# Performance work log

Measured on AMD Instinct MI355X. Metric: run time of the kernel, lower is better.

Reference implementation:

```python
import jax, jax.numpy as jnp
import numpy as np

N = 50_000      # nodes
E = 1_600_000   # edges (avg degree 32)
IN = 128        # in_channels
H = 128         # hidden_channels
OUT = 10        # out_channels
EA = 16         # edge_attr_channels


def setup_inputs() -> dict:
    key = jax.random.key(0)
    ks = jax.random.split(key, 16)
    def lin(k, fan_in, fan_out):
        return jax.random.normal(k, (fan_in, fan_out), dtype=jnp.float32) * (1.0 / np.sqrt(fan_in))
    return {
        "x": jax.random.normal(ks[0], (N, IN), dtype=jnp.float32),
        "edge_index": jax.random.randint(ks[1], (2, E), 0, N, dtype=jnp.int32),
        "edge_attr": jax.random.normal(ks[2], (E, EA), dtype=jnp.float32),
        # edge encoder MLP: Linear(EA->H) -> ReLU -> Linear(H->1)
        "We1": lin(ks[3], EA, H), "be1": jnp.zeros((H,), jnp.float32),
        "We2": lin(ks[4], H, 1),  "be2": jnp.zeros((1,), jnp.float32),
        # three GCNConv layers (in->H, H->H, H->H)
        "W1": lin(ks[5], IN, H), "b1": jnp.zeros((H,), jnp.float32),
        "W2": lin(ks[6], H, H),  "b2": jnp.zeros((H,), jnp.float32),
        "W3": lin(ks[7], H, H),  "b3": jnp.zeros((H,), jnp.float32),
        # head Linear(H->OUT)
        "Wh": lin(ks[8], H, OUT), "bh": jnp.zeros((OUT,), jnp.float32),
    }


def reference(x, edge_index, edge_attr, We1, be1, We2, be2,
              W1, b1, W2, b2, W3, b3, Wh, bh):
    n = x.shape[0]
    src, dst = edge_index[0], edge_index[1]

    # edge weight = softplus(MLP(edge_attr)).squeeze(-1)
    hidden = jax.nn.relu(edge_attr @ We1 + be1)          # [E, H]
    ew = jax.nn.softplus((hidden @ We2 + be2)[:, 0])      # [E]

    # add self-loops with weight 1 (GCNConv default)
    loops = jnp.arange(n, dtype=src.dtype)
    src_f = jnp.concatenate([src, loops])
    dst_f = jnp.concatenate([dst, loops])
    w_f = jnp.concatenate([ew, jnp.ones((n,), ew.dtype)])

    # symmetric normalization: D^{-1/2} A D^{-1/2}
    deg = jax.ops.segment_sum(w_f, dst_f, num_segments=n)   # [N]
    dis = jax.lax.rsqrt(jnp.maximum(deg, 1e-12))
    norm = dis[src_f] * w_f * dis[dst_f]                     # [E+N]

    def gcn_conv(h, W, b):
        h = h @ W                                             # [N, H]
        msg = norm[:, None] * h[src_f]                        # gather + scale
        agg = jax.ops.segment_sum(msg, dst_f, num_segments=n) # scatter-add
        return agg + b

    h = jax.nn.relu(gcn_conv(x, W1, b1))   # dropout is identity in eval
    h = jax.nn.relu(gcn_conv(h, W2, b2))
    h = jax.nn.relu(gcn_conv(h, W3, b3))

    graph_emb = jnp.mean(h, axis=0)        # global mean pool (single graph)
    return graph_emb @ Wh + bh             # [OUT], already squeezed
```

## Files before the change

kernel.cpp:

```cpp
#include <hip/hip_runtime.h>


#define HD   128
#define EAD  16
#define OUTD 10
#define PCHUNK 4096
#define PBLK 400

typedef short bf16x8 __attribute__((ext_vector_type(8)));
typedef float f32x16 __attribute__((ext_vector_type(16)));

static inline int ceil_div(long long a, long long b){ return (int)((a + b - 1) / b); }

__device__ inline unsigned f2bf(float f) {
    unsigned u = __float_as_uint(f);
    return (u + 0x7fffu + ((u >> 16) & 1u)) >> 16;
}
__device__ inline float bf_lo(unsigned w) { return __uint_as_float(w << 16); }
__device__ inline float bf_hi(unsigned w) { return __uint_as_float(w & 0xffff0000u); }

__device__ inline unsigned short f2h(float f) {
    _Float16 h = (_Float16)f;
    return __builtin_bit_cast(unsigned short, h);
}
__device__ inline float h2f(unsigned u) {
    _Float16 h = __builtin_bit_cast(_Float16, (unsigned short)(u & 0xffffu));
    return (float)h;
}
__device__ inline unsigned cvtpk(float lo, float hi) {
    unsigned r;
    asm volatile("v_cvt_pk_bf16_f32 %0, %1, %2" : "=v"(r) : "v"(lo), "v"(hi));
    return r;
}
__device__ inline unsigned relu_pk(unsigned w) {
    return w & ~(((w >> 15) & 0x10001u) * 0xFFFFu);
}
__device__ inline float softplus_fast(float v) {
    float t = __builtin_amdgcn_exp2f(-fabsf(v) * 1.44269504088896f);
    return fmaxf(v, 0.f) + 0.693147180559945f * __builtin_amdgcn_logf(1.0f + t);
}

__global__ __launch_bounds__(256) void k_edge_mlp(
    const float* __restrict__ edge_attr, const int* __restrict__ dst,
    const float* __restrict__ We1, const float* __restrict__ be1,
    const float* __restrict__ We2, const float* __restrict__ be2,
    float* __restrict__ ew, int* __restrict__ batom, int E, int NB)
{
    __shared__ int hist[256];
    const int tid = threadIdx.x;
    hist[tid] = 0;
    __syncthreads();

    const int lane = tid & 63;
    const int half = lane >> 5;
    const int lc   = lane & 31;
    const int wid  = blockIdx.x * 4 + (tid >> 6);
    const int nw   = gridDim.x * 4;
    const int G    = (E + 31) >> 5;

    bf16x8 bfr[4];
    bf16x8 abias[4];
    bf16x8 bones;
    bf16x8 we2A[8];
#pragma unroll
    for (int t = 0; t < 4; ++t) {
#pragma unroll
        for (int j = 0; j < 8; ++j) {
            int k = 4 * half + (j & 3) + 8 * (j >> 2);
            bfr[t][j]   = (short)f2bf(We1[k * HD + t * 32 + lc]);
            abias[t][j] = (half == 0 && j == 0) ? (short)f2bf(be1[t * 32 + lc]) : (short)0;
        }
    }
#pragma unroll
    for (int j = 0; j < 8; ++j)
        bones[j] = (half == 0 && j == 0) ? (short)0x3F80 : (short)0;
#pragma unroll
    for (int s = 0; s < 8; ++s)
#pragma unroll
        for (int j = 0; j < 8; ++j) {
            int k = 4 * half + (j & 3) + 8 * (j >> 2);
            we2A[s][j] = (short)f2bf(We2[s * 16 + k]);
        }
    const float be2v = be2[0];

    for (int g = wid * 2; g < G; g += nw * 2) {
        int g1 = g + 1;
        bool h1 = (g1 < G);
        int e0 = (g << 5) + lc;
        int e1 = h1 ? ((g1 << 5) + lc) : e0;
        int el0 = e0 < E ? e0 : E - 1;
        int el1 = e1 < E ? e1 : E - 1;
        bool own0 = (half == 0) && (e0 < E);
        bool own1 = h1 && (half == 0) && (e1 < E);
        if (own0) atomicAdd(&hist[((unsigned)dst[e0]) >> 8], 1);
        if (own1) atomicAdd(&hist[((unsigned)dst[e1]) >> 8], 1);

        const float4* r0 = reinterpret_cast<const float4*>(edge_attr + (size_t)el0 * EAD);
        const float4* r1 = reinterpret_cast<const float4*>(edge_attr + (size_t)el1 * EAD);
        float4 x00 = r0[half], x01 = r0[2 + half];
        float4 x10 = r1[half], x11 = r1[2 + half];
        union { uint2 u[2]; bf16x8 v; } af0, af1;
        af0.u[0] = make_uint2(cvtpk(x00.x, x00.y), cvtpk(x00.z, x00.w));
        af0.u[1] = make_uint2(cvtpk(x01.x, x01.y), cvtpk(x01.z, x01.w));
        af1.u[0] = make_uint2(cvtpk(x10.x, x10.y), cvtpk(x10.z, x10.w));
        af1.u[1] = make_uint2(cvtpk(x11.x, x11.y), cvtpk(x11.z, x11.w));

        f32x16 preA, preB;
#pragma unroll
        for (int i = 0; i < 16; ++i) { preA[i] = 0.f; preB[i] = 0.f; }
#pragma unroll
        for (int t = 0; t < 4; ++t) {
            f32x16 accA, accB;
#pragma unroll
            for (int i = 0; i < 16; ++i) { accA[i] = 0.f; accB[i] = 0.f; }
            accA = __builtin_amdgcn_mfma_f32_32x32x16_bf16(abias[t], bones, accA, 0, 0, 0);
            accB = __builtin_amdgcn_mfma_f32_32x32x16_bf16(abias[t], bones, accB, 0, 0, 0);
            accA = __builtin_amdgcn_mfma_f32_32x32x16_bf16(bfr[t], af0.v, accA, 0, 0, 0);
            accB = __builtin_amdgcn_mfma_f32_32x32x16_bf16(bfr[t], af1.v, accB, 0, 0, 0);
            union { uint2 u[2]; bf16x8 v; } ploA, phiA, ploB, phiB;
            ploA.u[0] = make_uint2(cvtpk(fmaxf(accA[0], 0.f),  fmaxf(accA[1], 0.f)),
                                   cvtpk(fmaxf(accA[2], 0.f),  fmaxf(accA[3], 0.f)));
            ploA.u[1] = make_uint2(cvtpk(fmaxf(accA[4], 0.f),  fmaxf(accA[5], 0.f)),
                                   cvtpk(fmaxf(accA[6], 0.f),  fmaxf(accA[7], 0.f)));
            phiA.u[0] = make_uint2(cvtpk(fmaxf(accA[8], 0.f),  fmaxf(accA[9], 0.f)),
                                   cvtpk(fmaxf(accA[10], 0.f), fmaxf(accA[11], 0.f)));
            phiA.u[1] = make_uint2(cvtpk(fmaxf(accA[12], 0.f), fmaxf(accA[13], 0.f)),
                                   cvtpk(fmaxf(accA[14], 0.f), fmaxf(accA[15], 0.f)));
            ploB.u[0] = make_uint2(cvtpk(fmaxf(accB[0], 0.f),  fmaxf(accB[1], 0.f)),
                                   cvtpk(fmaxf(accB[2], 0.f),  fmaxf(accB[3], 0.f)));
            ploB.u[1] = make_uint2(cvtpk(fmaxf(accB[4], 0.f),  fmaxf(accB[5], 0.f)),
                                   cvtpk(fmaxf(accB[6], 0.f),  fmaxf(accB[7], 0.f)));
            phiB.u[0] = make_uint2(cvtpk(fmaxf(accB[8], 0.f),  fmaxf(accB[9], 0.f)),
                                   cvtpk(fmaxf(accB[10], 0.f), fmaxf(accB[11], 0.f)));
            phiB.u[1] = make_uint2(cvtpk(fmaxf(accB[12], 0.f), fmaxf(accB[13], 0.f)),
                                   cvtpk(fmaxf(accB[14], 0.f), fmaxf(accB[15], 0.f)));
            preA = __builtin_amdgcn_mfma_f32_32x32x16_bf16(we2A[2*t],     ploA.v, preA, 0, 0, 0);
            preB = __builtin_amdgcn_mfma_f32_32x32x16_bf16(we2A[2*t],     ploB.v, preB, 0, 0, 0);
            preA = __builtin_amdgcn_mfma_f32_32x32x16_bf16(we2A[2*t + 1], phiA.v, preA, 0, 0, 0);
            preB = __builtin_amdgcn_mfma_f32_32x32x16_bf16(we2A[2*t + 1], phiB.v, preB, 0, 0, 0);
        }
        float v0 = preA[0] + be2v;
        float v1 = preB[0] + be2v;
        if (own0) ew[e0] = softplus_fast(v0);
        if (own1) ew[e1] = softplus_fast(v1);
    }
    __syncthreads();
    if (tid < NB && hist[tid]) atomicAdd(&batom[tid], hist[tid]);
}

__global__ __launch_bounds__(256) void k_bscan(
    const int* __restrict__ batom, int* __restrict__ boff,
    int* __restrict__ bcur, int NB)
{
    __shared__ int sh[256];
    int t = threadIdx.x;
    int v = (t < NB) ? batom[t] : 0;
    sh[t] = v;
    __syncthreads();
    for (int off = 1; off < 256; off <<= 1) {
        int add = (t >= off) ? sh[t - off] : 0;
        __syncthreads();
        sh[t] += add;
        __syncthreads();
    }
    if (t < NB) { boff[t] = sh[t] - v; bcur[t] = sh[t] - v; }
    if (t == NB - 1) boff[NB] = sh[t];
}

__global__ __launch_bounds__(256) void k_part(
    const int* __restrict__ src, const int* __restrict__ dst,
    const float* __restrict__ ew, int* __restrict__ bcur,
    uint2* __restrict__ bbuf, int E, int NB)
{
    __shared__ int hist[256];
    __shared__ int base[256];
    __shared__ int cur[256];
    int t = threadIdx.x;
    hist[t] = 0; cur[t] = 0;
    __syncthreads();
    int eb = blockIdx.x * PCHUNK;
#pragma unroll
    for (int k = 0; k < PCHUNK / 256; ++k) {
        int e = eb + k * 256 + t;
        if (e < E) atomicAdd(&hist[dst[e] >> 8], 1);
    }
    __syncthreads();
    if (t < NB && hist[t]) base[t] = atomicAdd(&bcur[t], hist[t]);
    __syncthreads();
#pragma unroll
    for (int k = 0; k < PCHUNK / 256; ++k) {
        int e = eb + k * 256 + t;
        if (e >= E) continue;
        int d = dst[e];
        int bkt = d >> 8;
        int pos = base[bkt] + atomicAdd(&cur[bkt], 1);
        bbuf[pos] = make_uint2(((unsigned)src[e] << 16) | f2h(ew[e]),
                               (unsigned)(d & 255));
    }
}

__global__ __launch_bounds__(256) void k_bucket(
    const int* __restrict__ boff, const uint2* __restrict__ bbuf,
    int* __restrict__ rp, float* __restrict__ dis,
    unsigned* __restrict__ adj, int N, int E, int NB)
{
    __shared__ int   hcnt[256];
    __shared__ int   hexc[256];
    __shared__ int   cur[256];
    __shared__ float degs[256];
    int b = blockIdx.x;
    int t = threadIdx.x;
    hcnt[t] = 0; cur[t] = 0; degs[t] = 0.f;
    __syncthreads();
    int beg = boff[b], end = boff[b + 1];
    for (int i = beg + t; i < end; i += 256) {
        uint2 ent = bbuf[i];
        int dl = (int)ent.y;
        atomicAdd(&hcnt[dl], 1);
        atomicAdd(&degs[dl], h2f(ent.x));
    }
    __syncthreads();
    {
        int v = hcnt[t];
        hexc[t] = v;
        __syncthreads();
        for (int off = 1; off < 256; off <<= 1) {
            int add = (t >= off) ? hexc[t - off] : 0;
            __syncthreads();
            hexc[t] += add;
            __syncthreads();
        }
        hexc[t] -= v;
    }
    int n = (b << 8) + t;
    if (n < N) {
        rp[n]  = beg + hexc[t];
        dis[n] = rsqrtf(fmaxf(1.0f + degs[t], 1e-12f));
    }
    if (b == NB - 1 && t == 0) rp[N] = E;
    __syncthreads();
    for (int i = beg + t; i < end; i += 256) {
        uint2 ent = bbuf[i];
        int dl = (int)ent.y;
        int pos = beg + hexc[dl] + atomicAdd(&cur[dl], 1);
        adj[pos] = ent.x;
    }
}

template <bool BF16IN, bool RELU>
__global__ __launch_bounds__(256) void k_gemm(
    const void* __restrict__ Xv, const float* __restrict__ W,
    const float* __restrict__ dis, unsigned short* __restrict__ Ybf, int N)
{
    __shared__ unsigned short Wt[128][132];
    int t = threadIdx.x;
#pragma unroll
    for (int i = 0; i < 64; ++i) {
        int e = i * 256 + t;
        int k = e >> 7, n = e & 127;
        Wt[n][k] = (unsigned short)f2bf(W[e]);
    }
    __syncthreads();

    const int lane = t & 63;
    const int half = lane >> 5;
    const int lc   = lane & 31;
    const int wid  = blockIdx.x * 4 + (t >> 6);
    const int nw   = gridDim.x * 4;
    const int T    = (N + 31) >> 5;

    for (int tile = wid; tile < T; tile += nw) {
        int rbase = tile << 5;
        int arow  = rbase + lc; if (arow >= N) arow = N - 1;

        f32x16 acc[4];
#pragma unroll
        for (int tb = 0; tb < 4; ++tb)
#pragma unroll
            for (int i = 0; i < 16; ++i) acc[tb][i] = 0.f;

#pragma unroll
        for (int kk = 0; kk < 8; ++kk) {
            union { uint2 u[2]; bf16x8 v; } af;
            if (BF16IN) {
                const unsigned short* Xb = (const unsigned short*)Xv;
                const unsigned short* rp = Xb + (size_t)arow * HD + kk * 16 + 4 * half;
                uint2 lo = *reinterpret_cast<const uint2*>(rp);
                uint2 hi = *reinterpret_cast<const uint2*>(rp + 8);
                if (RELU) {
                    lo.x = relu_pk(lo.x); lo.y = relu_pk(lo.y);
                    hi.x = relu_pk(hi.x); hi.y = relu_pk(hi.y);
                }
                af.u[0] = lo; af.u[1] = hi;
            } else {
                const float* Xf = (const float*)Xv;
                const float* rp = Xf + (size_t)arow * HD + kk * 16 + 4 * half;
                float4 lo = *reinterpret_cast<const float4*>(rp);
                float4 hi = *reinterpret_cast<const float4*>(rp + 8);
                af.u[0] = make_uint2(cvtpk(lo.x, lo.y), cvtpk(lo.z, lo.w));
                af.u[1] = make_uint2(cvtpk(hi.x, hi.y), cvtpk(hi.z, hi.w));
            }
#pragma unroll
            for (int tb = 0; tb < 4; ++tb) {
                const unsigned short* wp = &Wt[tb * 32 + lc][kk * 16 + 4 * half];
                union { uint2 u[2]; bf16x8 v; } bf_;
                bf_.u[0] = *reinterpret_cast<const uint2*>(wp);
                bf_.u[1] = *reinterpret_cast<const uint2*>(wp + 8);
                acc[tb] = __builtin_amdgcn_mfma_f32_32x32x16_bf16(af.v, bf_.v, acc[tb], 0, 0, 0);
            }
        }

        float disv = dis[arow];
#pragma unroll
        for (int r = 0; r < 16; ++r) {
            int rofs = (r & 3) + 8 * (r >> 2) + 4 * half;
            int grow = rbase + rofs;
            float d = __shfl(disv, rofs, 32);
            if (grow < N) {
#pragma unroll
                for (int tb = 0; tb < 4; ++tb)
                    Ybf[(size_t)grow * HD + tb * 32 + lc] =
                        (unsigned short)f2bf(acc[tb][r] * d);
            }
        }
    }
}

__global__ __launch_bounds__(256) void k_gather(
    const int* __restrict__ rp, const unsigned* __restrict__ adj,
    const unsigned* __restrict__ linbf, const float* __restrict__ dis,
    const float* __restrict__ b, unsigned short* __restrict__ out, int N)
{
    int n = blockIdx.x * 8 + (threadIdx.x >> 5);
    if (n >= N) return;
    int lane = threadIdx.x & 31;
    uint2 sw = *reinterpret_cast<const uint2*>(linbf + (size_t)n * (HD/2) + lane * 2);
    float4 acc;
    acc.x = bf_lo(sw.x); acc.y = bf_hi(sw.x);
    acc.z = bf_lo(sw.y); acc.w = bf_hi(sw.y);
    int beg = rp[n], end = rp[n + 1];
    for (int i0 = beg; i0 < end; i0 += 32) {
        int m = end - i0; if (m > 32) m = 32;
        unsigned a = 0;
        if (lane < m) a = adj[i0 + lane];
        int j = 0;
        for (; j + 16 <= m; j += 16) {
            unsigned ee[16]; uint2 vv[16];
#pragma unroll
            for (int q = 0; q < 16; ++q) ee[q] = __shfl(a, j + q, 32);
#pragma unroll
            for (int q = 0; q < 16; ++q)
                vv[q] = *reinterpret_cast<const uint2*>(linbf + (size_t)(ee[q] >> 16) * (HD/2) + lane * 2);
#pragma unroll
            for (int q = 0; q < 16; ++q) {
                float wq = h2f(ee[q]);
                acc.x = fmaf(wq, bf_lo(vv[q].x), acc.x);
                acc.y = fmaf(wq, bf_hi(vv[q].x), acc.y);
                acc.z = fmaf(wq, bf_lo(vv[q].y), acc.z);
                acc.w = fmaf(wq, bf_hi(vv[q].y), acc.w);
            }
        }
        for (; j + 8 <= m; j += 8) {
            unsigned ee[8]; uint2 vv[8];
#pragma unroll
            for (int q = 0; q < 8; ++q) ee[q] = __shfl(a, j + q, 32);
#pragma unroll
            for (int q = 0; q < 8; ++q)
                vv[q] = *reinterpret_cast<const uint2*>(linbf + (size_t)(ee[q] >> 16) * (HD/2) + lane * 2);
#pragma unroll
            for (int q = 0; q < 8; ++q) {
                float wq = h2f(ee[q]);
                acc.x = fmaf(wq, bf_lo(vv[q].x), acc.x);
                acc.y = fmaf(wq, bf_hi(vv[q].x), acc.y);
                acc.z = fmaf(wq, bf_lo(vv[q].y), acc.z);
                acc.w = fmaf(wq, bf_hi(vv[q].y), acc.w);
            }
        }
        for (; j < m; ++j) {
            unsigned e0 = __shfl(a, j, 32);
            uint2 v0 = *reinterpret_cast<const uint2*>(linbf + (size_t)(e0 >> 16) * (HD/2) + lane * 2);
            float w0 = h2f(e0);
            acc.x = fmaf(w0, bf_lo(v0.x), acc.x);
            acc.y = fmaf(w0, bf_hi(v0.x), acc.y);
            acc.z = fmaf(w0, bf_lo(v0.y), acc.z);
            acc.w = fmaf(w0, bf_hi(v0.y), acc.w);
        }
    }
    float dn = dis[n];
    float4 bv = reinterpret_cast<const float4*>(b)[lane];
    unsigned w0 = cvtpk(fmaf(dn, acc.x, bv.x), fmaf(dn, acc.y, bv.y));
    unsigned w1 = cvtpk(fmaf(dn, acc.z, bv.z), fmaf(dn, acc.w, bv.w));
    *reinterpret_cast<uint2*>(out + (size_t)n * HD + lane * 4) = make_uint2(w0, w1);
}

__global__ __launch_bounds__(256) void k_pool(
    const unsigned short* __restrict__ h, float* __restrict__ part, int N)
{
    __shared__ float sm[16][128];
    int t  = threadIdx.x;
    int cg = t & 15;
    int rs = t >> 4;
    float acc[8];
#pragma unroll
    for (int i = 0; i < 8; ++i) acc[i] = 0.f;
    for (int r = blockIdx.x * 16 + rs; r < N; r += gridDim.x * 16) {
        uint4 v = *reinterpret_cast<const uint4*>(h + (size_t)r * HD + cg * 8);
        acc[0] += fmaxf(bf_lo(v.x), 0.f);
        acc[1] += fmaxf(bf_hi(v.x), 0.f);
        acc[2] += fmaxf(bf_lo(v.y), 0.f);
        acc[3] += fmaxf(bf_hi(v.y), 0.f);
        acc[4] += fmaxf(bf_lo(v.z), 0.f);
        acc[5] += fmaxf(bf_hi(v.z), 0.f);
        acc[6] += fmaxf(bf_lo(v.w), 0.f);
        acc[7] += fmaxf(bf_hi(v.w), 0.f);
    }
#pragma unroll
    for (int i = 0; i < 8; ++i) sm[rs][cg * 8 + i] = acc[i];
    __syncthreads();
    if (t < 128) {
        float s = 0.f;
#pragma unroll
        for (int k = 0; k < 16; ++k) s += sm[k][t];
        part[blockIdx.x * HD + t] = s;
    }
}

__global__ __launch_bounds__(1024) void k_head(
    const float* __restrict__ part, const float* __restrict__ Wh,
    const float* __restrict__ bh, float* __restrict__ out, float invN)
{
    __shared__ float smc[8][128];
    __shared__ float col[HD];
    int t = threadIdx.x;
    {
        int c  = t & 127;
        int ch = t >> 7;
        float s0 = 0.f, s1 = 0.f;
        int k0 = ch * 50;
#pragma unroll
        for (int k = 0; k < 50; k += 2) {
            s0 += part[(k0 + k)     * HD + c];
            s1 += part[(k0 + k + 1) * HD + c];
        }
        smc[ch][c] = s0 + s1;
    }
    __syncthreads();
    if (t < 128) {
        float s = 0.f;
#pragma unroll
        for (int k = 0; k < 8; ++k) s += smc[k][t];
        col[t] = s * invN;
    }
    __syncthreads();
    {
        int o = t >> 6;
        int l = t & 63;
        if (o < OUTD) {
            float acc = col[l] * Wh[l * OUTD + o]
                      + col[l + 64] * Wh[(l + 64) * OUTD + o];
#pragma unroll
            for (int off = 1; off < 64; off <<= 1)
                acc += __shfl_xor(acc, off, 64);
            if (l == 0) out[o] = acc + bh[o];
        }
    }
}

extern "C" void kernel_launch(void* const* d_in, const int* in_sizes, int n_in,
                              void* d_out, int out_size, void* d_ws, size_t ws_size,
                              hipStream_t stream)
{
    const float* x         = (const float*)d_in[0];
    const int*   ei        = (const int*)  d_in[1];
    const float* edge_attr = (const float*)d_in[2];
    const float* We1       = (const float*)d_in[3];
    const float* be1       = (const float*)d_in[4];
    const float* We2       = (const float*)d_in[5];
    const float* be2       = (const float*)d_in[6];
    const float* W1        = (const float*)d_in[7];
    const float* b1        = (const float*)d_in[8];
    const float* W2        = (const float*)d_in[9];
    const float* b2        = (const float*)d_in[10];
    const float* W3        = (const float*)d_in[11];
    const float* b3        = (const float*)d_in[12];
    const float* Wh        = (const float*)d_in[13];
    const float* bh        = (const float*)d_in[14];

    const int N = in_sizes[0] / HD;
    const int E = in_sizes[2] / EAD;
    const int NB = (N + 255) >> 8;
    const int* srcp = ei;
    const int* dstp = ei + E;

    char* w = (char*)d_ws;
    float*          ew   = (float*)w;          w += (size_t)E * sizeof(float);
    float*          dis  = (float*)w;          w += (size_t)N * sizeof(float);
    unsigned short* Bbf  = (unsigned short*)w; w += (size_t)N * HD * sizeof(unsigned short);
    unsigned*       Abf  = (unsigned*)w;       w += (size_t)N * (HD/2) * sizeof(unsigned);
    float*          part = (float*)w;          w += (size_t)PBLK * HD * sizeof(float);
    int*            rp   = (int*)w;            w += (size_t)(N + 2) * sizeof(int);
    int*            batom= (int*)w;            w += 256 * sizeof(int);
    int*            boff = (int*)w;            w += 260 * sizeof(int);
    int*            bcur = (int*)w;            w += 256 * sizeof(int);
    w = (char*)(((uintptr_t)w + 15) & ~(uintptr_t)15);
    uint2*          bbuf = (uint2*)w;          w += (size_t)E * sizeof(uint2);
    unsigned*       adj  = (unsigned*)w;       w += (size_t)E * sizeof(unsigned);

    const int gGe   = ceil_div(N, 8);
    const int gPart = ceil_div(E, PCHUNK);
    const int gGemm = 196;

    hipMemsetAsync(batom, 0, 256 * sizeof(int), stream);
    k_edge_mlp<<<1024, 256, 0, stream>>>(edge_attr, dstp, We1, be1, We2, be2,
                                         ew, batom, E, NB);

    k_bscan <<<1, 256, 0, stream>>>(batom, boff, bcur, NB);
    k_part  <<<gPart, 256, 0, stream>>>(srcp, dstp, ew, bcur, bbuf, E, NB);
    k_bucket<<<NB, 256, 0, stream>>>(boff, bbuf, rp, dis, adj, N, E, NB);

    k_gemm<false, false><<<gGemm, 256, 0, stream>>>(x, W1, dis, (unsigned short*)Abf, N);
    k_gather<<<gGe, 256, 0, stream>>>(rp, adj, Abf, dis, b1, Bbf, N);
    k_gemm<true, true><<<gGemm, 256, 0, stream>>>(Bbf, W2, dis, (unsigned short*)Abf, N);
    k_gather<<<gGe, 256, 0, stream>>>(rp, adj, Abf, dis, b2, Bbf, N);
    k_gemm<true, true><<<gGemm, 256, 0, stream>>>(Bbf, W3, dis, (unsigned short*)Abf, N);
    k_gather<<<gGe, 256, 0, stream>>>(rp, adj, Abf, dis, b3, Bbf, N);

    k_pool<<<PBLK, 256, 0, stream>>>(Bbf, part, N);
    k_head<<<1, 1024, 0, stream>>>(part, Wh, bh, (float*)d_out, 1.0f / (float)N);
}
```

Baseline: 373.2 us.

## Split feature dimension into four column slices for cache-resident gathers

```diff
diff --git a/kernel.cpp b/kernel.cpp
--- a/kernel.cpp
+++ b/kernel.cpp
@@ -18,6 +18,7 @@
 }
 __device__ inline float bf_lo(unsigned w) { return __uint_as_float(w << 16); }
 __device__ inline float bf_hi(unsigned w) { return __uint_as_float(w & 0xffff0000u); }
+__device__ inline float bf1(unsigned short u) { return __uint_as_float(((unsigned)u) << 16); }
 
 __device__ inline unsigned short f2h(float f) {
     _Float16 h = (_Float16)f;
@@ -319,7 +320,7 @@
             if (grow < N) {
 #pragma unroll
                 for (int tb = 0; tb < 4; ++tb)
-                    Ybf[(size_t)grow * HD + tb * 32 + lc] =
+                    Ybf[(size_t)tb * ((size_t)N * 32) + (size_t)grow * 32 + lc] =
                         (unsigned short)f2bf(acc[tb][r] * d);
             }
         }
@@ -328,69 +329,39 @@
 
 __global__ __launch_bounds__(256) void k_gather(
     const int* __restrict__ rp, const unsigned* __restrict__ adj,
-    const unsigned* __restrict__ linbf, const float* __restrict__ dis,
-    const float* __restrict__ b, unsigned short* __restrict__ out, int N)
+    const unsigned short* __restrict__ linbf, const float* __restrict__ dis,
+    const float* __restrict__ b, unsigned short* __restrict__ out,
+    int N, int pass)
 {
     int n = blockIdx.x * 8 + (threadIdx.x >> 5);
     if (n >= N) return;
     int lane = threadIdx.x & 31;
-    uint2 sw = *reinterpret_cast<const uint2*>(linbf + (size_t)n * (HD/2) + lane * 2);
-    float4 acc;
-    acc.x = bf_lo(sw.x); acc.y = bf_hi(sw.x);
-    acc.z = bf_lo(sw.y); acc.w = bf_hi(sw.y);
+    const unsigned short* sl = linbf + (size_t)pass * ((size_t)N * 32);
+    float acc = bf1(sl[(size_t)n * 32 + lane]);
     int beg = rp[n], end = rp[n + 1];
     for (int i0 = beg; i0 < end; i0 += 32) {
         int m = end - i0; if (m > 32) m = 32;
         unsigned a = 0;
         if (lane < m) a = adj[i0 + lane];
         int j = 0;
-        for (; j + 16 <= m; j += 16) {
-            unsigned ee[16]; uint2 vv[16];
-#pragma unroll
-            for (int q = 0; q < 16; ++q) ee[q] = __shfl(a, j + q, 32);
-#pragma unroll
-            for (int q = 0; q < 16; ++q)
-                vv[q] = *reinterpret_cast<const uint2*>(linbf + (size_t)(ee[q] >> 16) * (HD/2) + lane * 2);
-#pragma unroll
-            for (int q = 0; q < 16; ++q) {
-                float wq = h2f(ee[q]);
-                acc.x = fmaf(wq, bf_lo(vv[q].x), acc.x);
-                acc.y = fmaf(wq, bf_hi(vv[q].x), acc.y);
-                acc.z = fmaf(wq, bf_lo(vv[q].y), acc.z);
-                acc.w = fmaf(wq, bf_hi(vv[q].y), acc.w);
-            }
-        }
         for (; j + 8 <= m; j += 8) {
-            unsigned ee[8]; uint2 vv[8];
+            unsigned ee[8]; unsigned short vv[8];
 #pragma unroll
             for (int q = 0; q < 8; ++q) ee[q] = __shfl(a, j + q, 32);
 #pragma unroll
             for (int q = 0; q < 8; ++q)
-                vv[q] = *reinterpret_cast<const uint2*>(linbf + (size_t)(ee[q] >> 16) * (HD/2) + lane * 2);
-#pragma unroll
-            for (int q = 0; q < 8; ++q) {
-                float wq = h2f(ee[q]);
-                acc.x = fmaf(wq, bf_lo(vv[q].x), acc.x);
-                acc.y = fmaf(wq, bf_hi(vv[q].x), acc.y);
-                acc.z = fmaf(wq, bf_lo(vv[q].y), acc.z);
-                acc.w = fmaf(wq, bf_hi(vv[q].y), acc.w);
-            }
+                vv[q] = sl[(size_t)(ee[q] >> 16) * 32 + lane];
+#pragma unroll
+            for (int q = 0; q < 8; ++q)
+                acc = fmaf(h2f(ee[q]), bf1(vv[q]), acc);
         }
         for (; j < m; ++j) {
             unsigned e0 = __shfl(a, j, 32);
-            uint2 v0 = *reinterpret_cast<const uint2*>(linbf + (size_t)(e0 >> 16) * (HD/2) + lane * 2);
-            float w0 = h2f(e0);
-            acc.x = fmaf(w0, bf_lo(v0.x), acc.x);
-            acc.y = fmaf(w0, bf_hi(v0.x), acc.y);
-            acc.z = fmaf(w0, bf_lo(v0.y), acc.z);
-            acc.w = fmaf(w0, bf_hi(v0.y), acc.w);
-        }
-    }
-    float dn = dis[n];
-    float4 bv = reinterpret_cast<const float4*>(b)[lane];
-    unsigned w0 = cvtpk(fmaf(dn, acc.x, bv.x), fmaf(dn, acc.y, bv.y));
-    unsigned w1 = cvtpk(fmaf(dn, acc.z, bv.z), fmaf(dn, acc.w, bv.w));
-    *reinterpret_cast<uint2*>(out + (size_t)n * HD + lane * 4) = make_uint2(w0, w1);
+            acc = fmaf(h2f(e0), bf1(sl[(size_t)(e0 >> 16) * 32 + lane]), acc);
+        }
+    }
+    float r = fmaf(dis[n], acc, b[pass * 32 + lane]);
+    out[(size_t)n * HD + pass * 32 + lane] = (unsigned short)f2bf(r);
 }
 
 __global__ __launch_bounds__(256) void k_pool(
@@ -496,7 +467,7 @@
     float*          ew   = (float*)w;          w += (size_t)E * sizeof(float);
     float*          dis  = (float*)w;          w += (size_t)N * sizeof(float);
     unsigned short* Bbf  = (unsigned short*)w; w += (size_t)N * HD * sizeof(unsigned short);
-    unsigned*       Abf  = (unsigned*)w;       w += (size_t)N * (HD/2) * sizeof(unsigned);
+    unsigned short* Abf  = (unsigned short*)w; w += (size_t)N * HD * sizeof(unsigned short);
     float*          part = (float*)w;          w += (size_t)PBLK * HD * sizeof(float);
     int*            rp   = (int*)w;            w += (size_t)(N + 2) * sizeof(int);
     int*            batom= (int*)w;            w += 256 * sizeof(int);
@@ -518,12 +489,15 @@
     k_part  <<<gPart, 256, 0, stream>>>(srcp, dstp, ew, bcur, bbuf, E, NB);
     k_bucket<<<NB, 256, 0, stream>>>(boff, bbuf, rp, dis, adj, N, E, NB);
 
-    k_gemm<false, false><<<gGemm, 256, 0, stream>>>(x, W1, dis, (unsigned short*)Abf, N);
-    k_gather<<<gGe, 256, 0, stream>>>(rp, adj, Abf, dis, b1, Bbf, N);
-    k_gemm<true, true><<<gGemm, 256, 0, stream>>>(Bbf, W2, dis, (unsigned short*)Abf, N);
-    k_gather<<<gGe, 256, 0, stream>>>(rp, adj, Abf, dis, b2, Bbf, N);
-    k_gemm<true, true><<<gGemm, 256, 0, stream>>>(Bbf, W3, dis, (unsigned short*)Abf, N);
-    k_gather<<<gGe, 256, 0, stream>>>(rp, adj, Abf, dis, b3, Bbf, N);
+    k_gemm<false, false><<<gGemm, 256, 0, stream>>>(x, W1, dis, Abf, N);
+    for (int p = 0; p < 4; ++p)
+        k_gather<<<gGe, 256, 0, stream>>>(rp, adj, Abf, dis, b1, Bbf, N, p);
+    k_gemm<true, true><<<gGemm, 256, 0, stream>>>(Bbf, W2, dis, Abf, N);
+    for (int p = 0; p < 4; ++p)
+        k_gather<<<gGe, 256, 0, stream>>>(rp, adj, Abf, dis, b2, Bbf, N, p);
+    k_gemm<true, true><<<gGemm, 256, 0, stream>>>(Bbf, W3, dis, Abf, N);
+    for (int p = 0; p < 4; ++p)
+        k_gather<<<gGe, 256, 0, stream>>>(rp, adj, Abf, dis, b3, Bbf, N, p);
 
     k_pool<<<PBLK, 256, 0, stream>>>(Bbf, part, N);
     k_head<<<1, 1024, 0, stream>>>(part, Wh, bh, (float*)d_out, 1.0f / (float)N);
```

After: 447.8 us. 1.2x slower.
